# Kernel tuning notes

Hardware: AMD Instinct MI355X
Metric: run time of the kernel (lower is better)

## Reference

```python
import jax, jax.numpy as jnp
import numpy as np

B, N, D = 16384, 20, 13  # batch of states, agents per state, per-agent joint-state dim
SELF_STATE = 6           # self_state_size in SARL


def setup_inputs() -> dict:
    key = jax.random.key(0)
    ks = jax.random.split(key, 16)

    def init(k, fi, fo):
        # haiku MLP default: truncated-normal-ish std 1/sqrt(fan_in), zero bias
        return jax.random.normal(k, (fi, fo), jnp.float32) / np.float32(np.sqrt(fi))

    z = lambda n: jnp.zeros((n,), jnp.float32)
    return {
        "x": jax.random.normal(ks[0], (B, N, D), jnp.float32),
        # mlp1: 13 -> 150 -> 100, relu, activate_final=True
        "w1a": init(ks[1], D, 150), "b1a": z(150),
        "w1b": init(ks[2], 150, 100), "b1b": z(100),
        # attention: 200 -> 100 -> 100 -> 1
        "wa0": init(ks[3], 200, 100), "ba0": z(100),
        "wa1": init(ks[4], 100, 100), "ba1": z(100),
        "wa2": init(ks[5], 100, 1), "ba2": z(1),
        # mlp2: 100 -> 100 -> 50
        "w2a": init(ks[6], 100, 100), "b2a": z(100),
        "w2b": init(ks[7], 100, 50), "b2b": z(50),
        # mlp3: 56 -> 150 -> 100 -> 100 -> 1
        "w3a": init(ks[8], SELF_STATE + 50, 150), "b3a": z(150),
        "w3b": init(ks[9], 150, 100), "b3b": z(100),
        "w3c": init(ks[10], 100, 100), "b3c": z(100),
        "w3d": init(ks[11], 100, 1), "b3d": z(1),
    }


def reference(x, w1a, b1a, w1b, b1b, wa0, ba0, wa1, ba1, wa2, ba2,
              w2a, b2a, w2b, b2b, w3a, b3a, w3b, b3b, w3c, b3c, w3d, b3d):
    relu = jax.nn.relu
    # mlp1 (activate_final=True): [B,N,100]
    h1 = relu(relu(x @ w1a + b1a) @ w1b + b1b)
    # mean-pool over agents -> global state, broadcast + concat: [B,N,200]
    g = jnp.mean(h1, axis=1, keepdims=True)
    att_in = jnp.concatenate([h1, jnp.broadcast_to(g, h1.shape)], axis=-1)
    # attention MLP -> scores [B,N], softmax over agents
    s = relu(att_in @ wa0 + ba0)
    s = relu(s @ wa1 + ba1)
    scores = (s @ wa2 + ba2)[..., 0]
    attn = jax.nn.softmax(scores, axis=-1)
    # mlp2 features [B,N,50], softmax-weighted sum over agents -> [B,50]
    f = relu(h1 @ w2a + b2a) @ w2b + b2b
    wf = jnp.einsum('bnf,bn->bf', f, attn)
    # concat self-state (first row's first 6 dims) with pooled features -> [B,56]
    self_state = x[:, 0, :SELF_STATE]
    m = jnp.concatenate([self_state, wf], axis=-1)
    # mlp3: 56 -> 150 -> 100 -> 100 -> 1
    h = relu(m @ w3a + b3a)
    h = relu(h @ w3b + b3b)
    h = relu(h @ w3c + b3c)
    return h @ w3d + b3d  # [B,1] state value
```

## Files before the change

### kernel.cpp

```cpp
#include <hip/hip_runtime.h>
#include <math.h>

#define NT     512
#define NWAVES 8
#define GB     4
#define NTOK   20
#define NTT_P  5

typedef _Float16 f16x8 __attribute__((ext_vector_type(8)));
typedef _Float16 f16x4 __attribute__((ext_vector_type(4)));
typedef _Float16 f16x2 __attribute__((ext_vector_type(2)));
typedef float    f32x4 __attribute__((ext_vector_type(4)));

#define WS_W1A  0
#define WS_W1B  5120
#define WS_WA0  23040
#define WS_WA1  37376
#define WS_W2A  51712
#define WS_W2B  66048
#define WS_W3A  74240
#define WS_W3B  84480
#define WS_W3C  102400
#define WS_WA0H 116736
#define WS_TOTAL 131072
#define WB_BASE 65536
#define WB_B1A  0
#define WB_B1B  160
#define WB_BA0  272
#define WB_BA1  384
#define WB_B2A  496
#define WB_B2B  608
#define WB_B3A  672
#define WB_B3B  832
#define WB_B3C  944
#define WB_WA2  1056
#define WB_N    1168
#define PREP_TOTAL (WS_TOTAL + WB_N)
#define WS_MV   135168

#define LH_A    0
#define LH_B    12160
#define LH_C    23040
#define LH_T1   LH_A
#define LH_S1   LH_A
#define LH_F1   LH_A
#define LH_H1   LH_B
#define LH_FF   LH_B
#define LH_GQ   LH_C
#define LF_PART 11520
#define LF_GB   12672
#define LF_ATT  13120
#define LF_SS   13200
#define LDS_DW  13224
#define LDS_BYTES (LDS_DW * 4)

#define TB      64
#define TL_MV   0
#define TL_HA   4096
#define TL_HB   14848
#define TL_HC   23552
#define LDS_T_DW   16128
#define LDS_T_BYTES (LDS_T_DW * 4)

__device__ __forceinline__ void prep_one(const float* __restrict__ src, _Float16* dst,
                                         int local, int N, int K, int Ks)
{
    int n = local / Ks, k = local - n * Ks;
    dst[local] = (_Float16)((n < N && k < K) ? src[k * N + n] : 0.f);
}
__device__ __forceinline__ void prep_b(const float* __restrict__ src, float* dst,
                                       int idx, int N)
{
    dst[idx] = (idx < N) ? src[idx] : 0.f;
}

__global__ __launch_bounds__(256)
void prep_kernel(const float* __restrict__ w1a, const float* __restrict__ w1b,
                 const float* __restrict__ wa0, const float* __restrict__ wa1,
                 const float* __restrict__ w2a, const float* __restrict__ w2b,
                 const float* __restrict__ w3a, const float* __restrict__ w3b,
                 const float* __restrict__ w3c, const float* __restrict__ wa2,
                 const float* __restrict__ b1a, const float* __restrict__ b1b,
                 const float* __restrict__ ba0, const float* __restrict__ ba1,
                 const float* __restrict__ b2a, const float* __restrict__ b2b,
                 const float* __restrict__ b3a, const float* __restrict__ b3b,
                 const float* __restrict__ b3c,
                 _Float16* __restrict__ ws)
{
    int g = blockIdx.x * 256 + threadIdx.x;
    if (g >= PREP_TOTAL) return;
    if (g >= WS_TOTAL) {
        float* wb = (float*)ws + WB_BASE;
        int l = g - WS_TOTAL;
        if (l < WB_B1B)      prep_b(b1a, wb + WB_B1A, l - WB_B1A, 150);
        else if (l < WB_BA0) prep_b(b1b, wb + WB_B1B, l - WB_B1B, 100);
        else if (l < WB_BA1) prep_b(ba0, wb + WB_BA0, l - WB_BA0, 100);
        else if (l < WB_B2A) prep_b(ba1, wb + WB_BA1, l - WB_BA1, 100);
        else if (l < WB_B2B) prep_b(b2a, wb + WB_B2A, l - WB_B2A, 100);
        else if (l < WB_B3A) prep_b(b2b, wb + WB_B2B, l - WB_B2B, 50);
        else if (l < WB_B3B) prep_b(b3a, wb + WB_B3A, l - WB_B3A, 150);
        else if (l < WB_B3C) prep_b(b3b, wb + WB_B3B, l - WB_B3B, 100);
        else if (l < WB_WA2) prep_b(b3c, wb + WB_B3C, l - WB_B3C, 100);
        else                 prep_b(wa2, wb + WB_WA2, l - WB_WA2, 100);
        return;
    }
    if (g < WS_W1B)       prep_one(w1a, ws + WS_W1A, g - WS_W1A, 150, 13, 32);
    else if (g < WS_WA0)  prep_one(w1b, ws + WS_W1B, g - WS_W1B, 100, 150, 160);
    else if (g < WS_WA1)  prep_one(wa0, ws + WS_WA0, g - WS_WA0, 100, 100, 128);
    else if (g < WS_W2A)  prep_one(wa1, ws + WS_WA1, g - WS_WA1, 100, 100, 128);
    else if (g < WS_W2B)  prep_one(w2a, ws + WS_W2A, g - WS_W2A, 100, 100, 128);
    else if (g < WS_W3A)  prep_one(w2b, ws + WS_W2B, g - WS_W2B,  50, 100, 128);
    else if (g < WS_W3B)  prep_one(w3a, ws + WS_W3A, g - WS_W3A, 150,  56, 64);
    else if (g < WS_W3C)  prep_one(w3b, ws + WS_W3B, g - WS_W3B, 100, 150, 160);
    else if (g < WS_WA0H) prep_one(w3c, ws + WS_W3C, g - WS_W3C, 100, 100, 128);
    else                  prep_one(wa0 + 100 * 100, ws + WS_WA0H, g - WS_WA0H, 100, 100, 128);
}

template<int KT, int MTL, int NTT, bool RELU, int BMODE, int OMODE, int CLW, int NW>
__device__ __forceinline__ void gemm_sw(const _Float16* X, const int Xs,
                                        const _Float16* __restrict__ WT, const int Bs,
                                        const float* __restrict__ biasp,
                                        const float* gbias,
                                        _Float16* Y, const int Ys,
                                        float* part, const float* __restrict__ wa2p,
                                        const int wv, const int lane)
{
    const int cl = lane & 15, kq = lane >> 4;
    constexpr int IPW = (MTL + NW - 1) / NW;
    f16x8 wf[IPW][KT];
    f32x4 bv[IPW];
#pragma unroll
    for (int ii = 0; ii < IPW; ++ii) {
        const int mt = wv + ii * NW;
        if (mt < MTL) {
            const _Float16* Wp = WT + (mt * 16 + cl) * Bs + kq * 8;
#pragma unroll
            for (int kt = 0; kt < KT; ++kt) wf[ii][kt] = *(const f16x8*)(Wp + kt * 32);
            if (BMODE == 0)
                bv[ii] = *(const f32x4*)(biasp + mt * 16 + kq * 4);
        }
    }
#pragma unroll
    for (int ii = 0; ii < IPW; ++ii) {
        const int mt = wv + ii * NW;
        if (mt >= MTL) break;
        const int fb = mt * 16 + kq * 4;
#pragma unroll
        for (int nt = 0; nt < NTT; ++nt) {
            const _Float16* Xp = X + (nt * 16 + cl) * Xs + kq * 8;
            f16x8 xf[KT];
#pragma unroll
            for (int kt = 0; kt < KT; ++kt) xf[kt] = *(const f16x8*)(Xp + kt * 32);
            f32x4 acc = {0.f, 0.f, 0.f, 0.f};
#pragma unroll
            for (int kt = 0; kt < KT; ++kt)
                acc = __builtin_amdgcn_mfma_f32_16x16x32_f16(wf[ii][kt], xf[kt], acc, 0, 0, 0);
            const int token = nt * 16 + cl;
            if (OMODE == 1) {
                if (cl < GB) {
                    f32x4 o = acc + bv[ii];
                    *(f32x4*)((float*)Y + cl * 112 + fb) = o;
                }
            } else if (OMODE == 2) {
                f32x4 y = acc + bv[ii];
                y[0] = fmaxf(y[0], 0.f); y[1] = fmaxf(y[1], 0.f);
                y[2] = fmaxf(y[2], 0.f); y[3] = fmaxf(y[3], 0.f);
                f32x4 w4 = *(const f32x4*)(wa2p + fb);
                float p = y[0] * w4[0] + y[1] * w4[1] + y[2] * w4[2] + y[3] * w4[3];
                p += __shfl_xor(p, 16);
                p += __shfl_xor(p, 32);
                if (kq == 0) part[token * 8 + mt] = p;
            } else {
                f32x4 bb;
                if (BMODE == 1)
                    bb = *(const f32x4*)(gbias + (token / NTOK) * 112 + fb);
                else
                    bb = bv[ii];
                f32x4 y = acc + bb;
                if (RELU) {
                    y[0] = fmaxf(y[0], 0.f); y[1] = fmaxf(y[1], 0.f);
                    y[2] = fmaxf(y[2], 0.f); y[3] = fmaxf(y[3], 0.f);
                }
                if (fb < CLW) {
                    f16x4 o = { (_Float16)y[0], (_Float16)y[1],
                                (_Float16)y[2], (_Float16)y[3] };
                    *(f16x4*)(Y + token * Ys + fb) = o;
                }
            }
        }
    }
}

__global__ __launch_bounds__(NT, 6)
void vnet_kernel(const float* __restrict__ x,
                 const float* __restrict__ ba2,
                 const _Float16* __restrict__ wsh,
                 _Float16* __restrict__ mvg)
{
    extern __shared__ float lds_f[];
    _Float16* lds_h = (_Float16*)lds_f;

    const int tid  = threadIdx.x;
    const int lane = tid & 63, wv = tid >> 6;
    const int b0   = blockIdx.x * GB;
    const float* wb = (const float*)wsh + WB_BASE;

    _Float16* xa  = lds_h + LH_C;
    _Float16* gqh = lds_h + LH_GQ;
    _Float16* h1w = lds_h + LH_H1;
    float* gbias = lds_f + LF_GB;
    float* att   = lds_f + LF_ATT;
    float* ss    = lds_f + LF_SS;
    float* part  = lds_f + LF_PART;

    const float* xg = x + (size_t)b0 * (NTOK * 13);
    for (int t = tid; t < GB * NTOK * 13; t += NT) {
        int row = t / 13, d = t - row * 13;
        xa[row * 40 + d] = (_Float16)xg[t];
    }
    for (int t = tid; t < 80 * 27; t += NT) {
        int row = t / 27, c = 13 + (t - row * 27);
        xa[row * 40 + c] = (_Float16)0.f;
    }
    for (int t = tid; t < 80 * 24; t += NT) {
        int row = t / 24, c = 112 + (t - row * 24);
        h1w[row * 136 + c] = (_Float16)0.f;
    }
    if (tid < 8) h1w[tid] = (_Float16)0.f;
    if (tid < GB * 6) {
        int b = tid / 6, d = tid - b * 6;
        ss[tid] = xg[b * (NTOK * 13) + d];
    }
    __syncthreads();

    gemm_sw<1, 10, NTT_P, true, 0, 0, 152, 8>(xa, 40, wsh + WS_W1A, 32,
        wb + WB_B1A, nullptr, lds_h + LH_T1, 152, nullptr, nullptr, wv, lane);
    __syncthreads();

    gemm_sw<5, 7, NTT_P, true, 0, 0, 10000, 8>(lds_h + LH_T1, 152, wsh + WS_W1B,
        160, wb + WB_B1B, nullptr, h1w, 136, nullptr, nullptr, wv, lane);
    __syncthreads();

    const _Float16* h1 = h1w;
    const uint* h1u = (const uint*)h1;
    for (int t = tid; t < GB * 50; t += NT) {
        int b = t / 50, cp = t - b * 50;
        float s0 = 0.f, s1 = 0.f;
#pragma unroll
        for (int n = 0; n < NTOK; ++n) {
            uint v = h1u[(b * NTOK + n) * 68 + cp];
            f16x2 p = *(const f16x2*)&v;
            s0 += (float)p.x; s1 += (float)p.y;
        }
        f16x2 g = { (_Float16)(s0 * 0.05f), (_Float16)(s1 * 0.05f) };
        *(f16x2*)(gqh + b * 136 + 2 * cp) = g;
    }
    __syncthreads();

    gemm_sw<4, 7, 1, false, 0, 1, 10000, 8>(gqh, 136, wsh + WS_WA0H, 128,
        wb + WB_BA0, nullptr, (_Float16*)gbias, 0, nullptr, nullptr, wv, lane);
    __syncthreads();

    gemm_sw<4, 7, NTT_P, true, 1, 0, 10000, 8>(h1, 136, wsh + WS_WA0, 128,
        nullptr, gbias, lds_h + LH_S1, 136, nullptr, nullptr, wv, lane);
    __syncthreads();

    gemm_sw<4, 7, NTT_P, true, 0, 2, 10000, 8>(lds_h + LH_S1, 136, wsh + WS_WA1,
        128, wb + WB_BA1, nullptr, nullptr, 0, part, wb + WB_WA2, wv, lane);
    __syncthreads();

    gemm_sw<4, 7, NTT_P, true, 0, 0, 10000, 8>(h1, 136, wsh + WS_W2A, 128,
        wb + WB_B2A, nullptr, lds_h + LH_F1, 136, nullptr, nullptr, wv, lane);
    __syncthreads();

    if (wv < 4) {
        gemm_sw<4, 4, NTT_P, false, 0, 0, 10000, 4>(lds_h + LH_F1, 136,
            wsh + WS_W2B, 128, wb + WB_B2B, nullptr, lds_h + LH_FF, 72,
            nullptr, nullptr, wv, lane);
    } else {
        const int b = wv - 4;
        float sc = -1e30f;
        if (lane < NTOK) {
            sc = ba2[0];
            const float* pr = part + (b * NTOK + lane) * 8;
#pragma unroll
            for (int m = 0; m < 7; ++m) sc += pr[m];
        }
        float mx = sc;
#pragma unroll
        for (int off = 16; off; off >>= 1) mx = fmaxf(mx, __shfl_xor(mx, off, 32));
        float e = (lane < NTOK) ? expf(sc - mx) : 0.f;
        float s = e;
#pragma unroll
        for (int off = 16; off; off >>= 1) s += __shfl_xor(s, off, 32);
        if (lane < NTOK) att[b * NTOK + lane] = e / s;
    }
    __syncthreads();

    const _Float16* fh = lds_h + LH_FF;
    for (int t = tid; t < GB * 64; t += NT) {
        int b = t >> 6, c = t & 63;
        float v = 0.f;
        if (c < 6) {
            v = ss[b * 6 + c];
        } else if (c < 56) {
            const int cc = c - 6;
            const float* ab = att + b * NTOK;
            float acc = 0.f;
#pragma unroll
            for (int n = 0; n < NTOK; ++n)
                acc = fmaf((float)fh[(b * NTOK + n) * 72 + cc], ab[n], acc);
            v = acc;
        }
        mvg[(size_t)(b0 + b) * 64 + c] = (_Float16)v;
    }
}

__global__ __launch_bounds__(NT)
void tail_kernel(const _Float16* __restrict__ mvg,
                 const float* __restrict__ w3d, const float* __restrict__ b3d,
                 const _Float16* __restrict__ wsh,
                 float* __restrict__ outp)
{
    extern __shared__ float lds_f[];
    _Float16* lds_h = (_Float16*)lds_f;

    const int tid  = threadIdx.x;
    const int lane = tid & 63, wv = tid >> 6;
    const int g0   = blockIdx.x * TB;
    const float* wb = (const float*)wsh + WB_BASE;

    _Float16* mvT = lds_h + TL_MV;
    {
        const uint* src = (const uint*)(mvg + (size_t)g0 * 64);
        uint* dst = (uint*)mvT;
        for (int t = tid; t < TB * 32; t += NT) dst[t] = src[t];
    }
    for (int t = tid; t < (TL_HC - TL_HB) / 2; t += NT)
        ((uint*)(lds_h + TL_HB))[t] = 0u;
    __syncthreads();

    gemm_sw<2, 10, 4, true, 0, 0, 10000, 8>(mvT, 64, wsh + WS_W3A, 64,
        wb + WB_B3A, nullptr, lds_h + TL_HA, 168, nullptr, nullptr, wv, lane);
    __syncthreads();

    gemm_sw<5, 7, 4, true, 0, 0, 10000, 8>(lds_h + TL_HA, 168, wsh + WS_W3B,
        160, wb + WB_B3B, nullptr, lds_h + TL_HB, 136, nullptr, nullptr, wv, lane);
    __syncthreads();

    gemm_sw<4, 7, 4, true, 0, 0, 10000, 8>(lds_h + TL_HB, 136, wsh + WS_W3C,
        128, wb + WB_B3C, nullptr, lds_h + TL_HC, 136, nullptr, nullptr, wv, lane);
    __syncthreads();

    {
        const int b = tid >> 3, kl = tid & 7;
        const _Float16* hc = lds_h + TL_HC + b * 136;
        float acc = 0.f;
#pragma unroll 13
        for (int k = kl; k < 100; k += 8)
            acc = fmaf((float)hc[k], w3d[k], acc);
        acc += __shfl_xor(acc, 1);
        acc += __shfl_xor(acc, 2);
        acc += __shfl_xor(acc, 4);
        if (kl == 0) outp[g0 + b] = acc + b3d[0];
    }
}

extern "C" void kernel_launch(void* const* d_in, const int* in_sizes, int n_in,
                              void* d_out, int out_size, void* d_ws, size_t ws_size,
                              hipStream_t stream)
{
    const float* x   = (const float*)d_in[0];
    const float* w1a = (const float*)d_in[1];
    const float* b1a = (const float*)d_in[2];
    const float* w1b = (const float*)d_in[3];
    const float* b1b = (const float*)d_in[4];
    const float* wa0 = (const float*)d_in[5];
    const float* ba0 = (const float*)d_in[6];
    const float* wa1 = (const float*)d_in[7];
    const float* ba1 = (const float*)d_in[8];
    const float* wa2 = (const float*)d_in[9];
    const float* ba2 = (const float*)d_in[10];
    const float* w2a = (const float*)d_in[11];
    const float* b2a = (const float*)d_in[12];
    const float* w2b = (const float*)d_in[13];
    const float* b2b = (const float*)d_in[14];
    const float* w3a = (const float*)d_in[15];
    const float* b3a = (const float*)d_in[16];
    const float* w3b = (const float*)d_in[17];
    const float* b3b = (const float*)d_in[18];
    const float* w3c = (const float*)d_in[19];
    const float* b3c = (const float*)d_in[20];
    const float* w3d = (const float*)d_in[21];
    const float* b3d = (const float*)d_in[22];
    float* outp = (float*)d_out;
    _Float16* wsh = (_Float16*)d_ws;
    _Float16* mvg = wsh + WS_MV;

    hipFuncSetAttribute((const void*)vnet_kernel,
                        hipFuncAttributeMaxDynamicSharedMemorySize, LDS_BYTES);
    hipFuncSetAttribute((const void*)tail_kernel,
                        hipFuncAttributeMaxDynamicSharedMemorySize, LDS_T_BYTES);

    hipLaunchKernelGGL(prep_kernel, dim3((PREP_TOTAL + 255) / 256), dim3(256),
                       0, stream,
                       w1a, w1b, wa0, wa1, w2a, w2b, w3a, w3b, w3c, wa2,
                       b1a, b1b, ba0, ba1, b2a, b2b, b3a, b3b, b3c, wsh);

    const int B = 16384;
    hipLaunchKernelGGL(vnet_kernel, dim3(B / GB), dim3(NT), LDS_BYTES, stream,
                       x, ba2, wsh, mvg);
    hipLaunchKernelGGL(tail_kernel, dim3(B / TB), dim3(NT), LDS_T_BYTES, stream,
                       mvg, w3d, b3d, wsh, outp);
}
```

Measured before the change: 119.6 us.

## Prefetch next layer's weights into registers during current GEMM phase

Splits the GEMM helper into a weight/bias register load and a compute step, so the next layer's weight fragments are fetched from global memory while the current layer's MFMAs run. A custom phase barrier waits only on LDS counters, which keeps those in-flight global loads from being drained at each sync. The tail kernel also pads the staged mv rows to a stride of 72 halfs to reduce LDS bank conflicts. In exchange, register pressure rises because two layers' weight fragments are live at once, which may lower occupancy under the launch bounds of 6 blocks.

```diff
diff --git a/kernel.cpp b/kernel.cpp
--- a/kernel.cpp
+++ b/kernel.cpp
@@ -11,6 +11,13 @@
 typedef _Float16 f16x4 __attribute__((ext_vector_type(4)));
 typedef _Float16 f16x2 __attribute__((ext_vector_type(2)));
 typedef float    f32x4 __attribute__((ext_vector_type(4)));
+
+#define PHASE_BAR() do {                                      \
+    asm volatile("s_waitcnt lgkmcnt(0)" ::: "memory");        \
+    __builtin_amdgcn_s_barrier();                             \
+    asm volatile("" ::: "memory");                            \
+    __builtin_amdgcn_sched_barrier(0);                        \
+} while (0)
 
 #define WS_W1A  0
 #define WS_W1B  5120
@@ -56,10 +63,10 @@
 
 #define TB      64
 #define TL_MV   0
-#define TL_HA   4096
-#define TL_HB   14848
-#define TL_HC   23552
-#define LDS_T_DW   16128
+#define TL_HA   4608
+#define TL_HB   15360
+#define TL_HC   24064
+#define LDS_T_DW   16384
 #define LDS_T_BYTES (LDS_T_DW * 4)
 
 __device__ __forceinline__ void prep_one(const float* __restrict__ src, _Float16* dst,
@@ -116,32 +123,43 @@
     else                  prep_one(wa0 + 100 * 100, ws + WS_WA0H, g - WS_WA0H, 100, 100, 128);
 }
 
-template<int KT, int MTL, int NTT, bool RELU, int BMODE, int OMODE, int CLW, int NW>
-__device__ __forceinline__ void gemm_sw(const _Float16* X, const int Xs,
-                                        const _Float16* __restrict__ WT, const int Bs,
-                                        const float* __restrict__ biasp,
-                                        const float* gbias,
-                                        _Float16* Y, const int Ys,
-                                        float* part, const float* __restrict__ wa2p,
-                                        const int wv, const int lane)
-{
-    const int cl = lane & 15, kq = lane >> 4;
-    constexpr int IPW = (MTL + NW - 1) / NW;
+template<int KT, int MTL, int NW>
+struct WC {
+    static constexpr int IPW = (MTL + NW - 1) / NW;
     f16x8 wf[IPW][KT];
     f32x4 bv[IPW];
-#pragma unroll
-    for (int ii = 0; ii < IPW; ++ii) {
+};
+
+template<int KT, int MTL, int NW, bool LOADB>
+__device__ __forceinline__ void load_w(WC<KT, MTL, NW>& W,
+                                       const _Float16* __restrict__ WT, const int Bs,
+                                       const float* __restrict__ biasp,
+                                       const int wv, const int lane)
+{
+    const int cl = lane & 15, kq = lane >> 4;
+#pragma unroll
+    for (int ii = 0; ii < WC<KT, MTL, NW>::IPW; ++ii) {
         const int mt = wv + ii * NW;
         if (mt < MTL) {
             const _Float16* Wp = WT + (mt * 16 + cl) * Bs + kq * 8;
 #pragma unroll
-            for (int kt = 0; kt < KT; ++kt) wf[ii][kt] = *(const f16x8*)(Wp + kt * 32);
-            if (BMODE == 0)
-                bv[ii] = *(const f32x4*)(biasp + mt * 16 + kq * 4);
-        }
-    }
-#pragma unroll
-    for (int ii = 0; ii < IPW; ++ii) {
+            for (int kt = 0; kt < KT; ++kt) W.wf[ii][kt] = *(const f16x8*)(Wp + kt * 32);
+            if (LOADB) W.bv[ii] = *(const f32x4*)(biasp + mt * 16 + kq * 4);
+        }
+    }
+}
+
+template<int KT, int MTL, int NTT, bool RELU, int BMODE, int OMODE, int CLW, int NW>
+__device__ __forceinline__ void gemm_c(const WC<KT, MTL, NW>& W,
+                                       const _Float16* X, const int Xs,
+                                       const float* gbias,
+                                       _Float16* Y, const int Ys,
+                                       float* part, const float* __restrict__ wa2p,
+                                       const int wv, const int lane)
+{
+    const int cl = lane & 15, kq = lane >> 4;
+#pragma unroll
+    for (int ii = 0; ii < WC<KT, MTL, NW>::IPW; ++ii) {
         const int mt = wv + ii * NW;
         if (mt >= MTL) break;
         const int fb = mt * 16 + kq * 4;
@@ -154,15 +172,15 @@
             f32x4 acc = {0.f, 0.f, 0.f, 0.f};
 #pragma unroll
             for (int kt = 0; kt < KT; ++kt)
-                acc = __builtin_amdgcn_mfma_f32_16x16x32_f16(wf[ii][kt], xf[kt], acc, 0, 0, 0);
+                acc = __builtin_amdgcn_mfma_f32_16x16x32_f16(W.wf[ii][kt], xf[kt], acc, 0, 0, 0);
             const int token = nt * 16 + cl;
             if (OMODE == 1) {
                 if (cl < GB) {
-                    f32x4 o = acc + bv[ii];
+                    f32x4 o = acc + W.bv[ii];
                     *(f32x4*)((float*)Y + cl * 112 + fb) = o;
                 }
             } else if (OMODE == 2) {
-                f32x4 y = acc + bv[ii];
+                f32x4 y = acc + W.bv[ii];
                 y[0] = fmaxf(y[0], 0.f); y[1] = fmaxf(y[1], 0.f);
                 y[2] = fmaxf(y[2], 0.f); y[3] = fmaxf(y[3], 0.f);
                 f32x4 w4 = *(const f32x4*)(wa2p + fb);
@@ -175,7 +193,7 @@
                 if (BMODE == 1)
                     bb = *(const f32x4*)(gbias + (token / NTOK) * 112 + fb);
                 else
-                    bb = bv[ii];
+                    bb = W.bv[ii];
                 f32x4 y = acc + bb;
                 if (RELU) {
                     y[0] = fmaxf(y[0], 0.f); y[1] = fmaxf(y[1], 0.f);
@@ -213,6 +231,15 @@
     float* ss    = lds_f + LF_SS;
     float* part  = lds_f + LF_PART;
 
+    WC<1, 10, 8> Wp2;
+    WC<5, 7, 8>  Wp3;
+    WC<4, 7, 8>  Wmg;
+    WC<4, 7, 8>  Wm1;
+    WC<4, 7, 8>  Wm2;
+    WC<4, 7, 8>  Wm3;
+    WC<4, 4, 4>  Wm4;
+
+    load_w<1, 10, 8, true>(Wp2, wsh + WS_W1A, 32, wb + WB_B1A, wv, lane);
     const float* xg = x + (size_t)b0 * (NTOK * 13);
     for (int t = tid; t < GB * NTOK * 13; t += NT) {
         int row = t / 13, d = t - row * 13;
@@ -231,16 +258,19 @@
         int b = tid / 6, d = tid - b * 6;
         ss[tid] = xg[b * (NTOK * 13) + d];
     }
-    __syncthreads();
-
-    gemm_sw<1, 10, NTT_P, true, 0, 0, 152, 8>(xa, 40, wsh + WS_W1A, 32,
-        wb + WB_B1A, nullptr, lds_h + LH_T1, 152, nullptr, nullptr, wv, lane);
-    __syncthreads();
-
-    gemm_sw<5, 7, NTT_P, true, 0, 0, 10000, 8>(lds_h + LH_T1, 152, wsh + WS_W1B,
-        160, wb + WB_B1B, nullptr, h1w, 136, nullptr, nullptr, wv, lane);
-    __syncthreads();
-
+    PHASE_BAR();
+
+    load_w<5, 7, 8, true>(Wp3, wsh + WS_W1B, 160, wb + WB_B1B, wv, lane);
+    gemm_c<1, 10, NTT_P, true, 0, 0, 152, 8>(Wp2, xa, 40, nullptr,
+        lds_h + LH_T1, 152, nullptr, nullptr, wv, lane);
+    PHASE_BAR();
+
+    load_w<4, 7, 8, true>(Wmg, wsh + WS_WA0H, 128, wb + WB_BA0, wv, lane);
+    gemm_c<5, 7, NTT_P, true, 0, 0, 10000, 8>(Wp3, lds_h + LH_T1, 152, nullptr,
+        h1w, 136, nullptr, nullptr, wv, lane);
+    PHASE_BAR();
+
+    load_w<4, 7, 8, false>(Wm1, wsh + WS_WA0, 128, nullptr, wv, lane);
     const _Float16* h1 = h1w;
     const uint* h1u = (const uint*)h1;
     for (int t = tid; t < GB * 50; t += NT) {
@@ -255,28 +285,30 @@
         f16x2 g = { (_Float16)(s0 * 0.05f), (_Float16)(s1 * 0.05f) };
         *(f16x2*)(gqh + b * 136 + 2 * cp) = g;
     }
-    __syncthreads();
-
-    gemm_sw<4, 7, 1, false, 0, 1, 10000, 8>(gqh, 136, wsh + WS_WA0H, 128,
-        wb + WB_BA0, nullptr, (_Float16*)gbias, 0, nullptr, nullptr, wv, lane);
-    __syncthreads();
-
-    gemm_sw<4, 7, NTT_P, true, 1, 0, 10000, 8>(h1, 136, wsh + WS_WA0, 128,
-        nullptr, gbias, lds_h + LH_S1, 136, nullptr, nullptr, wv, lane);
-    __syncthreads();
-
-    gemm_sw<4, 7, NTT_P, true, 0, 2, 10000, 8>(lds_h + LH_S1, 136, wsh + WS_WA1,
-        128, wb + WB_BA1, nullptr, nullptr, 0, part, wb + WB_WA2, wv, lane);
-    __syncthreads();
-
-    gemm_sw<4, 7, NTT_P, true, 0, 0, 10000, 8>(h1, 136, wsh + WS_W2A, 128,
-        wb + WB_B2A, nullptr, lds_h + LH_F1, 136, nullptr, nullptr, wv, lane);
-    __syncthreads();
+    PHASE_BAR();
+
+    load_w<4, 7, 8, true>(Wm2, wsh + WS_WA1, 128, wb + WB_BA1, wv, lane);
+    gemm_c<4, 7, 1, false, 0, 1, 10000, 8>(Wmg, gqh, 136, nullptr,
+        (_Float16*)gbias, 0, nullptr, nullptr, wv, lane);
+    PHASE_BAR();
+
+    load_w<4, 7, 8, true>(Wm3, wsh + WS_W2A, 128, wb + WB_B2A, wv, lane);
+    gemm_c<4, 7, NTT_P, true, 1, 0, 10000, 8>(Wm1, h1, 136, gbias,
+        lds_h + LH_S1, 136, nullptr, nullptr, wv, lane);
+    PHASE_BAR();
+
+    load_w<4, 4, 4, true>(Wm4, wsh + WS_W2B, 128, wb + WB_B2B, wv, lane);
+    gemm_c<4, 7, NTT_P, true, 0, 2, 10000, 8>(Wm2, lds_h + LH_S1, 136, nullptr,
+        nullptr, 0, part, wb + WB_WA2, wv, lane);
+    PHASE_BAR();
+
+    gemm_c<4, 7, NTT_P, true, 0, 0, 10000, 8>(Wm3, h1, 136, nullptr,
+        lds_h + LH_F1, 136, nullptr, nullptr, wv, lane);
+    PHASE_BAR();
 
     if (wv < 4) {
-        gemm_sw<4, 4, NTT_P, false, 0, 0, 10000, 4>(lds_h + LH_F1, 136,
-            wsh + WS_W2B, 128, wb + WB_B2B, nullptr, lds_h + LH_FF, 72,
-            nullptr, nullptr, wv, lane);
+        gemm_c<4, 4, NTT_P, false, 0, 0, 10000, 4>(Wm4, lds_h + LH_F1, 136,
+            nullptr, lds_h + LH_FF, 72, nullptr, nullptr, wv, lane);
     } else {
         const int b = wv - 4;
         float sc = -1e30f;
@@ -295,7 +327,7 @@
         for (int off = 16; off; off >>= 1) s += __shfl_xor(s, off, 32);
         if (lane < NTOK) att[b * NTOK + lane] = e / s;
     }
-    __syncthreads();
+    PHASE_BAR();
 
     const _Float16* fh = lds_h + LH_FF;
     for (int t = tid; t < GB * 64; t += NT) {
@@ -330,26 +362,34 @@
     const int g0   = blockIdx.x * TB;
     const float* wb = (const float*)wsh + WB_BASE;
 
+    WC<2, 10, 8> Wt1; WC<5, 7, 8> Wt2; WC<4, 7, 8> Wt3;
+    load_w<2, 10, 8, true>(Wt1, wsh + WS_W3A, 64, wb + WB_B3A, wv, lane);
+
     _Float16* mvT = lds_h + TL_MV;
     {
         const uint* src = (const uint*)(mvg + (size_t)g0 * 64);
         uint* dst = (uint*)mvT;
-        for (int t = tid; t < TB * 32; t += NT) dst[t] = src[t];
+        for (int t = tid; t < TB * 32; t += NT) {
+            int row = t >> 5, c = t & 31;
+            dst[row * 36 + c] = src[t];
+        }
     }
     for (int t = tid; t < (TL_HC - TL_HB) / 2; t += NT)
         ((uint*)(lds_h + TL_HB))[t] = 0u;
     __syncthreads();
 
-    gemm_sw<2, 10, 4, true, 0, 0, 10000, 8>(mvT, 64, wsh + WS_W3A, 64,
-        wb + WB_B3A, nullptr, lds_h + TL_HA, 168, nullptr, nullptr, wv, lane);
+    load_w<5, 7, 8, true>(Wt2, wsh + WS_W3B, 160, wb + WB_B3B, wv, lane);
+    gemm_c<2, 10, 4, true, 0, 0, 10000, 8>(Wt1, mvT, 72, nullptr,
+        lds_h + TL_HA, 168, nullptr, nullptr, wv, lane);
     __syncthreads();
 
-    gemm_sw<5, 7, 4, true, 0, 0, 10000, 8>(lds_h + TL_HA, 168, wsh + WS_W3B,
-        160, wb + WB_B3B, nullptr, lds_h + TL_HB, 136, nullptr, nullptr, wv, lane);
+    load_w<4, 7, 8, true>(Wt3, wsh + WS_W3C, 128, wb + WB_B3C, wv, lane);
+    gemm_c<5, 7, 4, true, 0, 0, 10000, 8>(Wt2, lds_h + TL_HA, 168, nullptr,
+        lds_h + TL_HB, 136, nullptr, nullptr, wv, lane);
     __syncthreads();
 
-    gemm_sw<4, 7, 4, true, 0, 0, 10000, 8>(lds_h + TL_HB, 136, wsh + WS_W3C,
-        128, wb + WB_B3C, nullptr, lds_h + TL_HC, 136, nullptr, nullptr, wv, lane);
+    gemm_c<4, 7, 4, true, 0, 0, 10000, 8>(Wt3, lds_h + TL_HB, 136, nullptr,
+        lds_h + TL_HC, 136, nullptr, nullptr, wv, lane);
     __syncthreads();
 
     {
```

New measurement: 133.9 us. 12.0% more time.
